# Kernel tuning notes

Hardware: AMD Instinct MI355X
Metric: run time of the kernel (lower is better)

Reference implementation:

```python
import jax, jax.numpy as jnp
import numpy as np

B, T, V, E, H, L = 32, 128, 32000, 1024, 1024, 3


def lstm_layer(x, Wx, Wh, b, h0, c0):
    """Standard LSTM (i,f,g,o gate order). x: [B,T,D]. Returns ([B,T,H], (h,c))."""
    def step(carry, xt):
        h, c = carry
        z = xt @ Wx + h @ Wh + b          # [B, 4H]
        i, f, g, o = jnp.split(z, 4, axis=-1)
        c = jax.nn.sigmoid(f) * c + jax.nn.sigmoid(i) * jnp.tanh(g)
        h = jax.nn.sigmoid(o) * jnp.tanh(c)
        return (h, c), h
    (h, c), ys = jax.lax.scan(step, (h0, c0), jnp.swapaxes(x, 0, 1))
    return jnp.swapaxes(ys, 0, 1), (h, c)


def setup_inputs() -> dict:
    key = jax.random.key(0)
    ks = jax.random.split(key, 12)
    s = 0.05  # small init to avoid gate saturation
    inp = {
        "enc_ids": jax.random.randint(ks[0], (B, T), 0, V, dtype=jnp.int32),
        "dec_ids": jax.random.randint(ks[1], (B, T), 0, V, dtype=jnp.int32),
        "emb": jax.random.normal(ks[2], (V, E), jnp.float32) * s,
        "Wx_enc": jax.random.normal(ks[3], (L, E, 4 * H), jnp.float32) * s,
        "Wh_enc": jax.random.normal(ks[4], (L, H, 4 * H), jnp.float32) * s,
        "b_enc": jnp.zeros((L, 4 * H), jnp.float32),
        "Wx_dec": jax.random.normal(ks[5], (L, E, 4 * H), jnp.float32) * s,
        "Wh_dec": jax.random.normal(ks[6], (L, H, 4 * H), jnp.float32) * s,
        "b_dec": jnp.zeros((L, 4 * H), jnp.float32),
        "dense_W": jax.random.normal(ks[7], (H, V), jnp.float32) * s,
        "dense_b": jnp.zeros((V,), jnp.float32),
    }
    return inp


def reference(enc_ids, dec_ids, emb, Wx_enc, Wh_enc, b_enc, Wx_dec, Wh_dec, b_dec, dense_W, dense_b):
    zeros = jnp.zeros((B, H), jnp.float32)
    # encoder: 3 stacked LSTMs, zero initial state each
    x = emb[enc_ids]                                      # [B,T,E]
    state = (zeros, zeros)
    for l in range(L):
        x, state = lstm_layer(x, Wx_enc[l], Wh_enc[l], b_enc[l], zeros, zeros)
    # decoder: faithful to source state chaining:
    # dec layer0 init = enc layer2 final; dec layer_{i+1} init = dec layer_i final
    y = emb[dec_ids]                                      # [B,T,E]
    for l in range(L):
        y, state = lstm_layer(y, Wx_dec[l], Wh_dec[l], b_dec[l], state[0], state[1])
    logits = y.reshape(-1, H) @ dense_W + dense_b          # [B*T, V]
    return logits.reshape(B, T, V)
```

## Files before the change

### kernel.cpp

```cpp
#include <hip/hip_runtime.h>


typedef __bf16 bf8 __attribute__((ext_vector_type(8)));
typedef float  f4  __attribute__((ext_vector_type(4)));

#define TLEN  128
#define HID   1024
#define G4    4096
#define VOC   32000
#define NBLK_SEQ 64

__device__ __forceinline__ ushort f2bf(float f) {
  unsigned u = __builtin_bit_cast(unsigned, f);
  u += 0x7fffu + ((u >> 16) & 1u);
  return (ushort)(u >> 16);
}
__device__ __forceinline__ float sigmoidf_(float x) { return 1.f / (1.f + expf(-x)); }

__device__ __forceinline__ void ld16_sys(uint4& v, const void* p) {
  asm volatile("global_load_dwordx4 %0, %1, off sc0 sc1" : "=v"(v) : "v"(p));
}
__device__ __forceinline__ unsigned ld4_sys(const void* p) {
  unsigned v;
  asm volatile("global_load_dword %0, %1, off sc0 sc1\n\ts_waitcnt vmcnt(0)"
               : "=v"(v) : "v"(p) : "memory");
  return v;
}
__device__ __forceinline__ void ld4_sys3(unsigned& a, unsigned& b, unsigned& c,
                                         const void* pa, const void* pb, const void* pc) {
  asm volatile("global_load_dword %0, %3, off sc0 sc1\n\t"
               "global_load_dword %1, %4, off sc0 sc1\n\t"
               "global_load_dword %2, %5, off sc0 sc1\n\t"
               "s_waitcnt vmcnt(0)"
               : "=&v"(a), "=&v"(b), "=&v"(c)
               : "v"(pa), "v"(pb), "v"(pc) : "memory");
}
__device__ __forceinline__ void st4_sys(void* p, unsigned v) {
  asm volatile("global_store_dword %0, %1, off sc0 sc1" :: "v"(p), "v"(v) : "memory");
}
__device__ __forceinline__ void wait_vm0() {
  asm volatile("s_waitcnt vmcnt(0)" ::: "memory");
  __builtin_amdgcn_sched_barrier(0);
}

typedef const __attribute__((address_space(1))) void GvoidC;
typedef __attribute__((address_space(3))) void Lvoid;
__device__ __forceinline__ void g2l16(const void* g, void* l) {
  __builtin_amdgcn_global_load_lds((GvoidC*)g, (Lvoid*)l, 16, 0, 0);
}

__global__ __launch_bounds__(256) void embed_kernel(const int* __restrict__ ids,
    const float* __restrict__ emb, ushort* __restrict__ out) {
  int r = blockIdx.x;
  int b = r & 31, t = r >> 5;
  int id = ids[b * TLEN + t];
  const float4* src = (const float4*)(emb + (size_t)id * HID);
  float4 v = src[threadIdx.x];
  ushort4 o;
  o.x = f2bf(v.x); o.y = f2bf(v.y); o.z = f2bf(v.z); o.w = f2bf(v.w);
  *(ushort4*)(out + (size_t)r * HID + threadIdx.x * 4) = o;
}

__global__ __launch_bounds__(256) void transpose_cvt(const float* __restrict__ W,
    ushort* __restrict__ Wt, int R, int C) {
  __shared__ float tile[32][33];
  int tx = threadIdx.x & 31, ty = threadIdx.x >> 5;
  int c0 = blockIdx.x * 32, r0 = blockIdx.y * 32;
  #pragma unroll
  for (int i = 0; i < 32; i += 8)
    tile[ty + i][tx] = W[(size_t)(r0 + ty + i) * C + c0 + tx];
  __syncthreads();
  #pragma unroll
  for (int i = 0; i < 32; i += 8)
    Wt[(size_t)(c0 + ty + i) * R + r0 + tx] = f2bf(tile[tx][ty + i]);
}

__global__ __launch_bounds__(256) void gemm_bt(const ushort* __restrict__ A,
    const ushort* __restrict__ Bt, const float* __restrict__ bias,
    float* __restrict__ C, int M, int N, int K, int permute) {
  __shared__ __align__(16) ushort lA[128 * 32];
  __shared__ __align__(16) ushort lB[128 * 32];
  int tid = threadIdx.x;
  int lane = tid & 63, wave = tid >> 6;
  int nwg = gridDim.x * gridDim.y;
  int wg  = blockIdx.y * gridDim.x + blockIdx.x;
  int q   = nwg >> 3;
  int swg = (wg & 7) * q + (wg >> 3);
  int m0 = (swg / gridDim.x) * 128, n0 = (swg % gridDim.x) * 128;
  int wr = wave >> 1, wc = wave & 1;
  f4 zero = {0.f, 0.f, 0.f, 0.f};
  f4 acc[4][4];
  #pragma unroll
  for (int i = 0; i < 4; i++)
    #pragma unroll
    for (int j = 0; j < 4; j++) acc[i][j] = zero;

  const ushort* Ag = A  + (size_t)(m0 + wave * 32 + (lane >> 2)) * K + (lane & 3) * 8;
  const ushort* Bg = Bt + (size_t)(n0 + wave * 32 + (lane >> 2)) * K + (lane & 3) * 8;
  ushort* lAp = lA + wave * 32 * 32;
  ushort* lBp = lB + wave * 32 * 32;

  for (int kt = 0; kt < K; kt += 32) {
    g2l16(Ag + kt, lAp);
    g2l16(Ag + (size_t)16 * K + kt, lAp + 16 * 32);
    g2l16(Bg + kt, lBp);
    g2l16(Bg + (size_t)16 * K + kt, lBp + 16 * 32);
    __syncthreads();
    bf8 aF[4], bF[4];
    #pragma unroll
    for (int i = 0; i < 4; i++)
      aF[i] = *(const bf8*)(lA + (wr * 64 + i * 16 + (lane & 15)) * 32 + (lane >> 4) * 8);
    #pragma unroll
    for (int j = 0; j < 4; j++)
      bF[j] = *(const bf8*)(lB + (wc * 64 + j * 16 + (lane & 15)) * 32 + (lane >> 4) * 8);
    #pragma unroll
    for (int i = 0; i < 4; i++)
      #pragma unroll
      for (int j = 0; j < 4; j++)
        acc[i][j] = __builtin_amdgcn_mfma_f32_16x16x32_bf16(aF[i], bF[j], acc[i][j], 0, 0, 0);
    __syncthreads();
  }
  #pragma unroll
  for (int i = 0; i < 4; i++) {
    #pragma unroll
    for (int j = 0; j < 4; j++) {
      int col = n0 + wc * 64 + j * 16 + (lane & 15);
      float bv = bias ? bias[col] : 0.f;
      #pragma unroll
      for (int v = 0; v < 4; v++) {
        int row = m0 + wr * 64 + i * 16 + (lane >> 4) * 4 + v;
        int orow = permute ? ((row & 31) * TLEN + (row >> 5)) : row;
        C[(size_t)orow * N + col] = acc[i][j][v] + bv;
      }
    }
  }
}

__global__ __launch_bounds__(512, 1) void enc_wave(
    const float*  __restrict__ Zpre,
    const ushort* __restrict__ WhT,
    const ushort* __restrict__ WxT,
    const float*  __restrict__ bE,
    ushort*       __restrict__ hxe,
    float*        __restrict__ cSe,
    ushort*       __restrict__ hS,
    unsigned*     __restrict__ flags)
{
  const int bx = blockIdx.x;
  const int l = bx >> 6, jg = bx & 63;
  const int j0 = jg * 16;
  const int tid = threadIdx.x;
  const int lane = tid & 63, wave = tid >> 6;
  const int g = wave & 3, op = wave >> 2;
  const int rr = tid >> 4, jj = tid & 15;

  __shared__ __align__(16) char hLDS[65536];
  __shared__ __align__(16) char xLDS[65536];
  __shared__ float zbuf[8][32][17];

  float cc = cSe[(size_t)l * 32768 + rr * HID + j0 + jj];
  float bias4[4];
  #pragma unroll
  for (int gg = 0; gg < 4; gg++)
    bias4[gg] = bE[l * G4 + gg * HID + j0 + jj];

  const bool mfma_on = (l > 0) || (op == 0);
  bf8 bw[32];
  if (mfma_on) {
    const ushort* Wb = op ? (WxT + (size_t)(l - 1) * G4 * HID)
                          : (WhT + (size_t)l * G4 * HID);
    const ushort* Bp = Wb + (size_t)(g * HID + j0 + (lane & 15)) * HID + (lane >> 4) * 8;
    #pragma unroll
    for (int kk = 0; kk < 32; kk++) bw[kk] = *(const bf8*)(Bp + kk * 32);
  }

  const int r0 = lane & 15, r1 = r0 + 16;
  const int klb = (lane >> 4) * 16;
  const int swz = (r0 & 7) << 4;

  float zv4[4], zn4[4];
  if (l == 0) {
    #pragma unroll
    for (int gg = 0; gg < 4; gg++)
      zv4[gg] = Zpre[(size_t)rr * G4 + gg * HID + j0 + jj];
  }

  for (int w = 0; w < 130; ++w) {
    if (w > 0) {
      if (wave == 0) {
        for (;;) {
          unsigned a, b, c;
          ld4_sys3(a, b, c, flags + lane * 4, flags + (64 + lane) * 4,
                   flags + (128 + lane) * 4);
          if (!__ballot(a < (unsigned)w || b < (unsigned)w || c < (unsigned)w)) break;
          __builtin_amdgcn_s_sleep(1);
        }
      }
      __syncthreads();
    }
    const int t = w - l;
    if (t >= 0 && t < TLEN) {
      const char* hsrc = (const char*)(hxe + ((size_t)l * 2 + ((t - 1) & 1)) * 32768);
      uint4 hreg[8], xreg[8];
      #pragma unroll
      for (int it = 0; it < 8; it++)
        ld16_sys(hreg[it], hsrc + (size_t)(tid + it * 512) * 16);
      if (l > 0) {
        const char* xsrc = (const char*)(hxe + ((size_t)(l - 1) * 2 + (t & 1)) * 32768);
        #pragma unroll
        for (int it = 0; it < 8; it++)
          ld16_sys(xreg[it], xsrc + (size_t)(tid + it * 512) * 16);
      }
      wait_vm0();
      #pragma unroll
      for (int it = 0; it < 8; it++) {
        int c = tid + it * 512;
        int row = c >> 7;
        int o = (c & 127) * 16;
        *(uint4*)(hLDS + row * 2048 + (o ^ ((row & 7) << 4))) = hreg[it];
      }
      if (l > 0) {
        #pragma unroll
        for (int it = 0; it < 8; it++) {
          int c = tid + it * 512;
          int row = c >> 7;
          int o = (c & 127) * 16;
          *(uint4*)(xLDS + row * 2048 + (o ^ ((row & 7) << 4))) = xreg[it];
        }
      }
      __syncthreads();

      if (l == 0 && t + 1 < TLEN) {
        const float* Ztn = Zpre + (size_t)(t + 1) * 32 * G4;
        #pragma unroll
        for (int gg = 0; gg < 4; gg++)
          zn4[gg] = Ztn[(size_t)rr * G4 + gg * HID + j0 + jj];
      }

      if (mfma_on) {
        const char* S = op ? xLDS : hLDS;
        f4 acc0 = {0.f, 0.f, 0.f, 0.f}, acc1 = {0.f, 0.f, 0.f, 0.f};
        #pragma unroll
        for (int kk = 0; kk < 32; kk++) {
          int cb = kk * 64 + klb;
          bf8 a0 = *(const bf8*)(S + r0 * 2048 + (cb ^ swz));
          bf8 a1 = *(const bf8*)(S + r1 * 2048 + (cb ^ swz));
          acc0 = __builtin_amdgcn_mfma_f32_16x16x32_bf16(a0, bw[kk], acc0, 0, 0, 0);
          acc1 = __builtin_amdgcn_mfma_f32_16x16x32_bf16(a1, bw[kk], acc1, 0, 0, 0);
        }
        #pragma unroll
        for (int v = 0; v < 4; v++) {
          zbuf[wave][(lane >> 4) * 4 + v][lane & 15]      = acc0[v];
          zbuf[wave][16 + (lane >> 4) * 4 + v][lane & 15] = acc1[v];
        }
      }
      __syncthreads();

      float z[4];
      #pragma unroll
      for (int gg = 0; gg < 4; gg++) z[gg] = zbuf[gg][rr][jj];
      if (l > 0) {
        #pragma unroll
        for (int gg = 0; gg < 4; gg++) z[gg] += zbuf[4 + gg][rr][jj] + bias4[gg];
      } else {
        #pragma unroll
        for (int gg = 0; gg < 4; gg++) z[gg] += zv4[gg];
        #pragma unroll
        for (int gg = 0; gg < 4; gg++) zv4[gg] = zn4[gg];
      }
      float ig = sigmoidf_(z[0]), fg = sigmoidf_(z[1]);
      float gv = tanhf(z[2]),     og = sigmoidf_(z[3]);
      cc = fg * cc + ig * gv;
      float hv = og * tanhf(cc);
      ushort hb = f2bf(hv);
      unsigned u = (unsigned)hb;
      unsigned nb = __shfl_xor(u, 1);
      if ((jj & 1) == 0)
        st4_sys(hxe + ((size_t)l * 2 + (t & 1)) * 32768 + rr * HID + j0 + jj,
                u | (nb << 16));
      if (t == TLEN - 1) {
        hS [(size_t)l * 32768 + rr * HID + j0 + jj] = hb;
        cSe[(size_t)l * 32768 + rr * HID + j0 + jj] = cc;
      }
      wait_vm0();
    }
    __syncthreads();
    if (tid == 0) st4_sys(flags + bx * 4, (unsigned)(w + 1));
  }
}

__global__ __launch_bounds__(256, 1) void lstm_seq(
    const float*  __restrict__ Zpre,
    const ushort* __restrict__ Wht,
    float*        __restrict__ cS,
    ushort*       __restrict__ yout,
    ushort*       __restrict__ hx,
    unsigned*     __restrict__ flags)
{
  const int jg = blockIdx.x;
  const int j0 = jg * 16;
  const int tid = threadIdx.x;
  const int lane = tid & 63, wave = tid >> 6;
  const int rr = tid >> 3, cp = tid & 7;

  __shared__ float zp[4][4][32][17];

  float2 cc = *(const float2*)(cS + (size_t)rr * HID + j0 + 2 * cp);

  bf8 bw[4][8];
  #pragma unroll
  for (int g = 0; g < 4; g++) {
    const ushort* Bp = Wht + (size_t)(g * HID + j0 + (lane & 15)) * HID
                     + wave * 256 + (lane >> 4) * 8;
    #pragma unroll
    for (int kk = 0; kk < 8; kk++)
      bw[g][kk] = *(const bf8*)(Bp + kk * 32);
  }

  const int r0 = lane & 15, r1 = r0 + 16;
  const int lk = lane >> 4;
  const int aoff0 = wave * 8192 + (lk >> 1) * 512 + r0 * 16 + (lk & 1) * 8;
  const int aoff1 = wave * 8192 + (lk >> 1) * 512 + r1 * 16 + (lk & 1) * 8;

  float2 zv[4], zn[4];
  #pragma unroll
  for (int g = 0; g < 4; g++)
    zv[g] = *(const float2*)(Zpre + (size_t)rr * G4 + g * HID + j0 + 2 * cp);

  for (int t = 0; t < TLEN; ++t) {
    if (t > 0) {
      if (wave == 0) {
        const unsigned* fp = flags + lane * 4;
        while (__ballot(ld4_sys(fp) < (unsigned)t)) __builtin_amdgcn_s_sleep(1);
      }
      __syncthreads();
    }
    const ushort* hsrc = hx + ((t + 1) & 1) * 32768;
    uint4 ha0[8], ha1[8];
    #pragma unroll
    for (int kk = 0; kk < 8; kk++) {
      ld16_sys(ha0[kk], hsrc + aoff0 + kk * 1024);
      ld16_sys(ha1[kk], hsrc + aoff1 + kk * 1024);
    }
    wait_vm0();

    if (t + 1 < TLEN) {
      const float* Ztn = Zpre + (size_t)(t + 1) * 32 * G4;
      #pragma unroll
      for (int g = 0; g < 4; g++)
        zn[g] = *(const float2*)(Ztn + (size_t)rr * G4 + g * HID + j0 + 2 * cp);
    }

    f4 acc0[4], acc1[4];
    #pragma unroll
    for (int g = 0; g < 4; g++) { acc0[g] = (f4){0,0,0,0}; acc1[g] = (f4){0,0,0,0}; }
    #pragma unroll
    for (int kk = 0; kk < 8; kk++) {
      bf8 a0 = __builtin_bit_cast(bf8, ha0[kk]);
      bf8 a1 = __builtin_bit_cast(bf8, ha1[kk]);
      #pragma unroll
      for (int g = 0; g < 4; g++) {
        acc0[g] = __builtin_amdgcn_mfma_f32_16x16x32_bf16(a0, bw[g][kk], acc0[g], 0, 0, 0);
        acc1[g] = __builtin_amdgcn_mfma_f32_16x16x32_bf16(a1, bw[g][kk], acc1[g], 0, 0, 0);
      }
    }
    #pragma unroll
    for (int g = 0; g < 4; g++)
      #pragma unroll
      for (int v = 0; v < 4; v++) {
        zp[wave][g][(lane >> 4) * 4 + v][lane & 15]      = acc0[g][v];
        zp[wave][g][16 + (lane >> 4) * 4 + v][lane & 15] = acc1[g][v];
      }
    __syncthreads();

    float zx[4], zy[4];
    #pragma unroll
    for (int g = 0; g < 4; g++) {
      zx[g] = zv[g].x + zp[0][g][rr][2 * cp]     + zp[1][g][rr][2 * cp]
                      + zp[2][g][rr][2 * cp]     + zp[3][g][rr][2 * cp];
      zy[g] = zv[g].y + zp[0][g][rr][2 * cp + 1] + zp[1][g][rr][2 * cp + 1]
                      + zp[2][g][rr][2 * cp + 1] + zp[3][g][rr][2 * cp + 1];
    }
    cc.x = sigmoidf_(zx[1]) * cc.x + sigmoidf_(zx[0]) * tanhf(zx[2]);
    cc.y = sigmoidf_(zy[1]) * cc.y + sigmoidf_(zy[0]) * tanhf(zy[2]);
    float hv0 = sigmoidf_(zx[3]) * tanhf(cc.x);
    float hv1 = sigmoidf_(zy[3]) * tanhf(cc.y);
    unsigned packed = (unsigned)f2bf(hv0) | ((unsigned)f2bf(hv1) << 16);
    *(unsigned*)(yout + (size_t)t * 32768 + rr * HID + j0 + 2 * cp) = packed;
    st4_sys(hx + (size_t)(t & 1) * 32768 + jg * 512 + rr * 16 + 2 * cp, packed);
    #pragma unroll
    for (int g = 0; g < 4; g++) zv[g] = zn[g];

    wait_vm0();
    __syncthreads();
    if (tid == 0) st4_sys(flags + jg * 4, (unsigned)(t + 1));
  }
  *(float2*)(cS + (size_t)rr * HID + j0 + 2 * cp) = cc;
}

__global__ __launch_bounds__(256) void prep_enc(ushort* hxe, float* cSe,
                                                unsigned* flags) {
  int i = blockIdx.x * 256 + threadIdx.x;
  hxe[i] = 0;
  if (i < 98304) cSe[i] = 0.f;
  if (i < 192)   flags[i * 4] = 0;
}
__global__ __launch_bounds__(256) void prep_dec0(const ushort* __restrict__ hS2,
                                                 const float* __restrict__ cSe2,
                                                 float* cS, ushort* hx,
                                                 unsigned* flags) {
  int i = blockIdx.x * 256 + threadIdx.x;
  int row = i >> 10, col = i & 1023;
  hx[32768 + (col >> 4) * 512 + row * 16 + (col & 15)] = hS2[i];
  cS[i] = cSe2[i];
  if (i < NBLK_SEQ) flags[i * 4] = 0;
}
__global__ __launch_bounds__(256) void prep_copy(const ushort* __restrict__ src,
                                                 ushort* __restrict__ hx,
                                                 unsigned* __restrict__ flags) {
  int i = blockIdx.x * 256 + threadIdx.x;
  int row = i >> 10, col = i & 1023;
  hx[32768 + (col >> 4) * 512 + row * 16 + (col & 15)] = src[i];
  if (i < NBLK_SEQ) flags[i * 4] = 0;
}

extern "C" void kernel_launch(void* const* d_in, const int* in_sizes, int n_in,
                              void* d_out, int out_size, void* d_ws, size_t ws_size,
                              hipStream_t stream) {
  const int*   enc_ids = (const int*)d_in[0];
  const int*   dec_ids = (const int*)d_in[1];
  const float* emb     = (const float*)d_in[2];
  const float* Wx_enc  = (const float*)d_in[3];
  const float* Wh_enc  = (const float*)d_in[4];
  const float* b_enc   = (const float*)d_in[5];
  const float* Wx_dec  = (const float*)d_in[6];
  const float* Wh_dec  = (const float*)d_in[7];
  const float* b_dec   = (const float*)d_in[8];
  const float* dense_W = (const float*)d_in[9];
  const float* dense_b = (const float*)d_in[10];
  float* out = (float*)d_out;

  char* ws = (char*)d_ws;
  const size_t SZ_BUF = (size_t)4096 * 1024 * 2;
  ushort*   bufA   = (ushort*)(ws);
  ushort*   bufB   = (ushort*)(ws + SZ_BUF);
  ushort*   Wxt    = (ushort*)(ws + 2 * SZ_BUF);
  ushort*   Wht    = (ushort*)(ws + 3 * SZ_BUF);
  ushort*   dWt    = (ushort*)(ws + 4 * SZ_BUF);
  char*     p2     = ws + 4 * SZ_BUF + (size_t)VOC * 1024 * 2;
  float*    cS     = (float*)(p2 + (size_t)32 * 1024 * 2);
  unsigned* flags  = (unsigned*)(p2 + (size_t)32 * 1024 * 2 + (size_t)32 * 1024 * 4);

  char* ob = (char*)d_out;
  float*    Zpre   = out;
  ushort*   WhTe   = (ushort*)(ob + (size_t)64  * 1024 * 1024);
  ushort*   WxTe   = (ushort*)(ob + (size_t)88  * 1024 * 1024);
  char*     st     = ob + (size_t)112 * 1024 * 1024;
  ushort*   hxe    = (ushort*)st;
  float*    cSe    = (float*)(st + 393216);
  ushort*   hS     = (ushort*)(st + 786432);
  unsigned* flags2 = (unsigned*)(st + 983040);
  ushort*   hxD    = (ushort*)(ob + (size_t)120 * 1024 * 1024);
  const size_t WSTRIDE = (size_t)G4 * HID;

  transpose_cvt<<<dim3(VOC / 32, 1024 / 32), 256, 0, stream>>>(dense_W, dWt, 1024, VOC);

  embed_kernel<<<4096, 256, 0, stream>>>(enc_ids, emb, bufA);
  transpose_cvt<<<dim3(G4 / 32, 32), 256, 0, stream>>>(Wx_enc, Wxt, 1024, G4);
  gemm_bt<<<dim3(G4 / 128, 4096 / 128), 256, 0, stream>>>(bufA, Wxt, b_enc,
                                                          Zpre, 4096, G4, 1024, 0);
  for (int l = 0; l < 3; l++)
    transpose_cvt<<<dim3(G4 / 32, 32), 256, 0, stream>>>(Wh_enc + (size_t)l * 1024 * G4,
                                                         WhTe + l * WSTRIDE, 1024, G4);
  for (int l = 1; l < 3; l++)
    transpose_cvt<<<dim3(G4 / 32, 32), 256, 0, stream>>>(Wx_enc + (size_t)l * 1024 * G4,
                                                         WxTe + (l - 1) * WSTRIDE, 1024, G4);
  prep_enc<<<768, 256, 0, stream>>>(hxe, cSe, flags2);
  enc_wave<<<192, 512, 0, stream>>>(Zpre, WhTe, WxTe, b_enc, hxe, cSe, hS, flags2);

  embed_kernel<<<4096, 256, 0, stream>>>(dec_ids, emb, bufA);
  ushort* cur = bufA; ushort* oth = bufB;
  for (int l = 0; l < 3; l++) {
    transpose_cvt<<<dim3(G4 / 32, 32), 256, 0, stream>>>(Wx_dec + (size_t)l * 1024 * G4, Wxt, 1024, G4);
    transpose_cvt<<<dim3(G4 / 32, 32), 256, 0, stream>>>(Wh_dec + (size_t)l * 1024 * G4, Wht, 1024, G4);
    gemm_bt<<<dim3(G4 / 128, 4096 / 128), 256, 0, stream>>>(cur, Wxt, b_dec + (size_t)l * G4,
                                                            Zpre, 4096, G4, 1024, 0);
    if (l == 0) {
      prep_dec0<<<128, 256, 0, stream>>>(hS + 2 * 32768, cSe + 2 * 32768, cS, hxD, flags);
    } else {
      const ushort* h0src = cur + (size_t)127 * 32 * HID;
      prep_copy<<<128, 256, 0, stream>>>(h0src, hxD, flags);
    }
    lstm_seq<<<NBLK_SEQ, 256, 0, stream>>>(Zpre, Wht, cS, oth, hxD, flags);
    ushort* tmp = cur; cur = oth; oth = tmp;
  }

  gemm_bt<<<dim3(VOC / 128, 4096 / 128), 256, 0, stream>>>(cur, dWt, dense_b, out,
                                                           4096, VOC, 1024, 1);
}
```

Baseline: 3.492 ms.

## Split encoder recurrent GEMM over K per wave and load h directly to registers

```diff
diff --git a/kernel.cpp b/kernel.cpp
--- a/kernel.cpp
+++ b/kernel.cpp
@@ -141,7 +141,7 @@
     const ushort* __restrict__ WhT,
     const ushort* __restrict__ WxT,
     const float*  __restrict__ bE,
-    ushort*       __restrict__ hxe,
+    ushort*       __restrict__ hxC,
     float*        __restrict__ cSe,
     ushort*       __restrict__ hS,
     unsigned*     __restrict__ flags)
@@ -151,38 +151,42 @@
   const int j0 = jg * 16;
   const int tid = threadIdx.x;
   const int lane = tid & 63, wave = tid >> 6;
-  const int g = wave & 3, op = wave >> 2;
+  const int op = wave >> 2, ks = wave & 3;
   const int rr = tid >> 4, jj = tid & 15;
 
-  __shared__ __align__(16) char hLDS[65536];
-  __shared__ __align__(16) char xLDS[65536];
-  __shared__ float zbuf[8][32][17];
+  __shared__ float zp[8][4][32][17];
 
   float cc = cSe[(size_t)l * 32768 + rr * HID + j0 + jj];
   float bias4[4];
   #pragma unroll
-  for (int gg = 0; gg < 4; gg++)
-    bias4[gg] = bE[l * G4 + gg * HID + j0 + jj];
+  for (int g = 0; g < 4; g++)
+    bias4[g] = bE[l * G4 + g * HID + j0 + jj];
 
   const bool mfma_on = (l > 0) || (op == 0);
-  bf8 bw[32];
+  bf8 bw[4][8];
   if (mfma_on) {
     const ushort* Wb = op ? (WxT + (size_t)(l - 1) * G4 * HID)
                           : (WhT + (size_t)l * G4 * HID);
-    const ushort* Bp = Wb + (size_t)(g * HID + j0 + (lane & 15)) * HID + (lane >> 4) * 8;
-    #pragma unroll
-    for (int kk = 0; kk < 32; kk++) bw[kk] = *(const bf8*)(Bp + kk * 32);
+    #pragma unroll
+    for (int g = 0; g < 4; g++) {
+      const ushort* Bp = Wb + (size_t)(g * HID + j0 + (lane & 15)) * HID
+                       + ks * 256 + (lane >> 4) * 8;
+      #pragma unroll
+      for (int kk = 0; kk < 8; kk++)
+        bw[g][kk] = *(const bf8*)(Bp + kk * 32);
+    }
   }
 
   const int r0 = lane & 15, r1 = r0 + 16;
-  const int klb = (lane >> 4) * 16;
-  const int swz = (r0 & 7) << 4;
+  const int lk = lane >> 4;
+  const int aoff0 = ks * 8192 + (lk >> 1) * 512 + r0 * 16 + (lk & 1) * 8;
+  const int aoff1 = ks * 8192 + (lk >> 1) * 512 + r1 * 16 + (lk & 1) * 8;
 
   float zv4[4], zn4[4];
   if (l == 0) {
     #pragma unroll
-    for (int gg = 0; gg < 4; gg++)
-      zv4[gg] = Zpre[(size_t)rr * G4 + gg * HID + j0 + jj];
+    for (int g = 0; g < 4; g++)
+      zv4[g] = Zpre[(size_t)rr * G4 + g * HID + j0 + jj];
   }
 
   for (int w = 0; w < 130; ++w) {
@@ -200,73 +204,65 @@
     }
     const int t = w - l;
     if (t >= 0 && t < TLEN) {
-      const char* hsrc = (const char*)(hxe + ((size_t)l * 2 + ((t - 1) & 1)) * 32768);
-      uint4 hreg[8], xreg[8];
-      #pragma unroll
-      for (int it = 0; it < 8; it++)
-        ld16_sys(hreg[it], hsrc + (size_t)(tid + it * 512) * 16);
-      if (l > 0) {
-        const char* xsrc = (const char*)(hxe + ((size_t)(l - 1) * 2 + (t & 1)) * 32768);
-        #pragma unroll
-        for (int it = 0; it < 8; it++)
-          ld16_sys(xreg[it], xsrc + (size_t)(tid + it * 512) * 16);
-      }
-      wait_vm0();
-      #pragma unroll
-      for (int it = 0; it < 8; it++) {
-        int c = tid + it * 512;
-        int row = c >> 7;
-        int o = (c & 127) * 16;
-        *(uint4*)(hLDS + row * 2048 + (o ^ ((row & 7) << 4))) = hreg[it];
-      }
-      if (l > 0) {
-        #pragma unroll
-        for (int it = 0; it < 8; it++) {
-          int c = tid + it * 512;
-          int row = c >> 7;
-          int o = (c & 127) * 16;
-          *(uint4*)(xLDS + row * 2048 + (o ^ ((row & 7) << 4))) = xreg[it];
+      uint4 ha0[8], ha1[8];
+      if (mfma_on) {
+        const ushort* src = (op == 0)
+          ? hxC + ((size_t)l * 2 + ((t - 1) & 1)) * 32768
+          : hxC + ((size_t)(l - 1) * 2 + (t & 1)) * 32768;
+        #pragma unroll
+        for (int kk = 0; kk < 8; kk++) {
+          ld16_sys(ha0[kk], src + aoff0 + kk * 1024);
+          ld16_sys(ha1[kk], src + aoff1 + kk * 1024);
         }
-      }
-      __syncthreads();
+        wait_vm0();
+      }
 
       if (l == 0 && t + 1 < TLEN) {
         const float* Ztn = Zpre + (size_t)(t + 1) * 32 * G4;
         #pragma unroll
-        for (int gg = 0; gg < 4; gg++)
-          zn4[gg] = Ztn[(size_t)rr * G4 + gg * HID + j0 + jj];
+        for (int g = 0; g < 4; g++)
+          zn4[g] = Ztn[(size_t)rr * G4 + g * HID + j0 + jj];
       }
 
       if (mfma_on) {
-        const char* S = op ? xLDS : hLDS;
-        f4 acc0 = {0.f, 0.f, 0.f, 0.f}, acc1 = {0.f, 0.f, 0.f, 0.f};
-        #pragma unroll
-        for (int kk = 0; kk < 32; kk++) {
-          int cb = kk * 64 + klb;
-          bf8 a0 = *(const bf8*)(S + r0 * 2048 + (cb ^ swz));
-          bf8 a1 = *(const bf8*)(S + r1 * 2048 + (cb ^ swz));
-          acc0 = __builtin_amdgcn_mfma_f32_16x16x32_bf16(a0, bw[kk], acc0, 0, 0, 0);
-          acc1 = __builtin_amdgcn_mfma_f32_16x16x32_bf16(a1, bw[kk], acc1, 0, 0, 0);
+        f4 acc0[4], acc1[4];
+        #pragma unroll
+        for (int g = 0; g < 4; g++) { acc0[g] = (f4){0,0,0,0}; acc1[g] = (f4){0,0,0,0}; }
+        #pragma unroll
+        for (int kk = 0; kk < 8; kk++) {
+          bf8 a0 = __builtin_bit_cast(bf8, ha0[kk]);
+          bf8 a1 = __builtin_bit_cast(bf8, ha1[kk]);
+          #pragma unroll
+          for (int g = 0; g < 4; g++) {
+            acc0[g] = __builtin_amdgcn_mfma_f32_16x16x32_bf16(a0, bw[g][kk], acc0[g], 0, 0, 0);
+            acc1[g] = __builtin_amdgcn_mfma_f32_16x16x32_bf16(a1, bw[g][kk], acc1[g], 0, 0, 0);
+          }
         }
         #pragma unroll
-        for (int v = 0; v < 4; v++) {
-          zbuf[wave][(lane >> 4) * 4 + v][lane & 15]      = acc0[v];
-          zbuf[wave][16 + (lane >> 4) * 4 + v][lane & 15] = acc1[v];
-        }
+        for (int g = 0; g < 4; g++)
+          #pragma unroll
+          for (int v = 0; v < 4; v++) {
+            zp[wave][g][(lane >> 4) * 4 + v][lane & 15]      = acc0[g][v];
+            zp[wave][g][16 + (lane >> 4) * 4 + v][lane & 15] = acc1[g][v];
+          }
       }
       __syncthreads();
 
       float z[4];
       #pragma unroll
-      for (int gg = 0; gg < 4; gg++) z[gg] = zbuf[gg][rr][jj];
-      if (l > 0) {
-        #pragma unroll
-        for (int gg = 0; gg < 4; gg++) z[gg] += zbuf[4 + gg][rr][jj] + bias4[gg];
-      } else {
-        #pragma unroll
-        for (int gg = 0; gg < 4; gg++) z[gg] += zv4[gg];
-        #pragma unroll
-        for (int gg = 0; gg < 4; gg++) zv4[gg] = zn4[gg];
+      for (int g = 0; g < 4; g++) {
+        float s = zp[0][g][rr][jj] + zp[1][g][rr][jj]
+                + zp[2][g][rr][jj] + zp[3][g][rr][jj];
+        if (l > 0)
+          s += zp[4][g][rr][jj] + zp[5][g][rr][jj]
+             + zp[6][g][rr][jj] + zp[7][g][rr][jj] + bias4[g];
+        else
+          s += zv4[g];
+        z[g] = s;
+      }
+      if (l == 0) {
+        #pragma unroll
+        for (int g = 0; g < 4; g++) zv4[g] = zn4[g];
       }
       float ig = sigmoidf_(z[0]), fg = sigmoidf_(z[1]);
       float gv = tanhf(z[2]),     og = sigmoidf_(z[3]);
@@ -276,7 +272,7 @@
       unsigned u = (unsigned)hb;
       unsigned nb = __shfl_xor(u, 1);
       if ((jj & 1) == 0)
-        st4_sys(hxe + ((size_t)l * 2 + (t & 1)) * 32768 + rr * HID + j0 + jj,
+        st4_sys(hxC + ((size_t)l * 2 + (t & 1)) * 32768 + jg * 512 + rr * 16 + jj,
                 u | (nb << 16));
       if (t == TLEN - 1) {
         hS [(size_t)l * 32768 + rr * HID + j0 + jj] = hb;
@@ -398,10 +394,10 @@
   *(float2*)(cS + (size_t)rr * HID + j0 + 2 * cp) = cc;
 }
 
-__global__ __launch_bounds__(256) void prep_enc(ushort* hxe, float* cSe,
+__global__ __launch_bounds__(256) void prep_enc(ushort* hxC, float* cSe,
                                                 unsigned* flags) {
   int i = blockIdx.x * 256 + threadIdx.x;
-  hxe[i] = 0;
+  hxC[i] = 0;
   if (i < 98304) cSe[i] = 0.f;
   if (i < 192)   flags[i * 4] = 0;
 }
@@ -456,7 +452,7 @@
   ushort*   WhTe   = (ushort*)(ob + (size_t)64  * 1024 * 1024);
   ushort*   WxTe   = (ushort*)(ob + (size_t)88  * 1024 * 1024);
   char*     st     = ob + (size_t)112 * 1024 * 1024;
-  ushort*   hxe    = (ushort*)st;
+  ushort*   hxC    = (ushort*)st;
   float*    cSe    = (float*)(st + 393216);
   ushort*   hS     = (ushort*)(st + 786432);
   unsigned* flags2 = (unsigned*)(st + 983040);
@@ -475,8 +471,8 @@
   for (int l = 1; l < 3; l++)
     transpose_cvt<<<dim3(G4 / 32, 32), 256, 0, stream>>>(Wx_enc + (size_t)l * 1024 * G4,
                                                          WxTe + (l - 1) * WSTRIDE, 1024, G4);
-  prep_enc<<<768, 256, 0, stream>>>(hxe, cSe, flags2);
-  enc_wave<<<192, 512, 0, stream>>>(Zpre, WhTe, WxTe, b_enc, hxe, cSe, hS, flags2);
+  prep_enc<<<768, 256, 0, stream>>>(hxC, cSe, flags2);
+  enc_wave<<<192, 512, 0, stream>>>(Zpre, WhTe, WxTe, b_enc, hxC, cSe, hS, flags2);
 
   embed_kernel<<<4096, 256, 0, stream>>>(dec_ids, emb, bufA);
   ushort* cur = bufA; ushort* oth = bufB;
```

Measured after the change: 3.160 ms. 9.5% less time.
